# Kernel optimization log

Measured on AMD Instinct MI355X. Metric: run time of the kernel, lower is better.

The kernel has to match this reference:

```python
import jax, jax.numpy as jnp
import numpy as np

N = 100000   # nodes
E = 3200000  # edges
M = 4096     # moves
K = 16       # orders per move
NEG_SLOPE = 0.2  # PyG GATv2Conv default negative_slope

PARAM_SHAPES = {
    'g1_Wl': (10, 15), 'g1_Wr': (10, 15), 'g1_att': (10,), 'g1_b': (10,),
    'g2_Wl': (10, 25), 'g2_Wr': (10, 25), 'g2_att': (10,), 'g2_b': (10,),
    'g3_Wl': (10, 25), 'g3_Wr': (10, 25), 'g3_att': (10,), 'g3_b': (10,),
    'vt_W': (20, 29), 'vt_b': (20,), 'va_W': (1, 20), 'va_b': (1,),
    'vv_W': (10, 20), 'vv_b': (10,), 'vl_W': (1, 10), 'vl_b': (1,),
    'at_W': (20, 48), 'at_b': (20,), 'dt_W': (20, 23), 'dt_b': (20,),
    'oa_W': (1, 20), 'oa_b': (1,), 'ov_W': (1, 20), 'ov_b': (1,),
}
PARAM_NAMES = list(PARAM_SHAPES.keys())


def _linear(x, W, b):
    return x @ W.T + b


def _gatv2(x, src, dst, Wl, Wr, att, b):
    # GATv2Conv (heads=1, self-loops appended by caller), eval mode (no dropout)
    xl = x @ Wl.T  # messages from source nodes
    xr = x @ Wr.T
    e = (jax.nn.leaky_relu(xl[src] + xr[dst], NEG_SLOPE) * att).sum(-1)  # [E+N]
    emax = jax.ops.segment_max(e, dst, num_segments=N)
    ee = jnp.exp(e - emax[dst])
    denom = jax.ops.segment_sum(ee, dst, num_segments=N)
    alpha = ee / denom[dst]
    return jax.ops.segment_sum(alpha[:, None] * xl[src], dst, num_segments=N) + b


def _forward(x1, x2, edges, move_src, move_dst, move_armies, is_attack, params):
    (g1_Wl, g1_Wr, g1_att, g1_b,
     g2_Wl, g2_Wr, g2_att, g2_b,
     g3_Wl, g3_Wr, g3_att, g3_b,
     vt_W, vt_b, va_W, va_b, vv_W, vv_b, vl_W, vl_b,
     at_W, at_b, dt_W, dt_b, oa_W, oa_b, ov_W, ov_b) = params
    x2t = jnp.tile(x2, (N, 1))  # [N,4]
    self_idx = jnp.arange(N, dtype=edges.dtype)
    src = jnp.concatenate([edges[0], self_idx])
    dst = jnp.concatenate([edges[1], self_idx])
    x = jax.nn.relu(_gatv2(x1, src, dst, g1_Wl, g1_Wr, g1_att, g1_b))
    x = jax.nn.relu(_gatv2(jnp.concatenate([x, x1], 1), src, dst, g2_Wl, g2_Wr, g2_att, g2_b))
    x = jax.nn.relu(_gatv2(jnp.concatenate([x, x1], 1), src, dst, g3_Wl, g3_Wr, g3_att, g3_b))  # [N,10]
    # per-move order tensors (vectorized over [M,K]); deploy uses move_src as target
    xs, xd = x[move_src], x[move_dst]       # [M,K,10]
    x1s, x1d = x1[move_src], x1[move_dst]   # [M,K,15]
    extra = 0.6 * move_armies - 0.7 * (x1d[..., 3] + x1d[..., 4])
    attack_in = jnp.concatenate([xs, xd, x1s[..., 3:], x1d[..., 1:],
                                 move_armies[..., None], extra[..., None]], -1)  # [M,K,48]
    deploy_in = jnp.concatenate([xs, x1s[..., 3:], move_armies[..., None]], -1)  # [M,K,23]
    feat = jnp.where(is_attack[..., None] == 1,
                     _linear(attack_in, at_W, at_b),
                     _linear(deploy_in, dt_W, dt_b))
    feat = jax.nn.relu(feat)  # dropout = identity (eval)
    attn = jax.nn.softmax(_linear(feat, oa_W, oa_b), axis=1)  # softmax over orders
    p = (attn * _linear(feat, ov_W, ov_b)).sum(axis=(1, 2))   # [M]
    # value head: attention pooling over all nodes
    Vn = jax.nn.relu(_linear(jnp.concatenate([x, x1, x2t], 1), vt_W, vt_b))  # [N,20]
    vatt = jax.nn.softmax(_linear(Vn, va_W, va_b), axis=0)
    Vp = jax.nn.relu((vatt * _linear(Vn, vv_W, vv_b)).sum(axis=0))
    V = jnp.tanh(_linear(Vp, vl_W, vl_b))[0]
    return V, jax.nn.log_softmax(p, axis=0)


def setup_inputs() -> dict:
    key = jax.random.key(0)
    ks = iter(jax.random.split(key, 64))
    inp = {
        'x1': jax.random.normal(next(ks), (N, 15), jnp.float32),
        'x2': jax.random.normal(next(ks), (4,), jnp.float32),
        'edges': jax.random.randint(next(ks), (2, E), 0, N, jnp.int32),
        'move_src': jax.random.randint(next(ks), (M, K), 0, N, jnp.int32),
        'move_dst': jax.random.randint(next(ks), (M, K), 0, N, jnp.int32),
        'move_armies': jax.random.uniform(next(ks), (M, K), jnp.float32) * 10.0,
        'is_attack': jax.random.randint(next(ks), (M, K), 0, 2, jnp.int32),
    }
    for name, shape in PARAM_SHAPES.items():
        inp[name] = jax.random.normal(next(ks), shape, jnp.float32) * 0.1
    return inp


def reference(x1, x2, edges, move_src, move_dst, move_armies, is_attack,
              g1_Wl, g1_Wr, g1_att, g1_b, g2_Wl, g2_Wr, g2_att, g2_b,
              g3_Wl, g3_Wr, g3_att, g3_b, vt_W, vt_b, va_W, va_b,
              vv_W, vv_b, vl_W, vl_b, at_W, at_b, dt_W, dt_b,
              oa_W, oa_b, ov_W, ov_b):
    params = (g1_Wl, g1_Wr, g1_att, g1_b, g2_Wl, g2_Wr, g2_att, g2_b,
              g3_Wl, g3_Wr, g3_att, g3_b, vt_W, vt_b, va_W, va_b,
              vv_W, vv_b, vl_W, vl_b, at_W, at_b, dt_W, dt_b,
              oa_W, oa_b, ov_W, ov_b)
    return _forward(x1, x2, edges, move_src, move_dst, move_armies, is_attack, params)
```

## Files before the change

kernel.cpp:

```cpp
#include <hip/hip_runtime.h>
#include <hip/hip_fp16.h>
#include <math.h>

#define NN 100000
#define NE 3200000
#define MM 4096
#define KK 16
#define NEG_SLOPE 0.2f
#define SUB 8
#define BSH 8
#define NB 391
#define PCH 4096
#define FCAP 9728
#define XS 12
#define XSH 16
#define PART_BLOCKS ((NE + NN + PCH - 1) / PCH)
#define LIN_BLOCKS  ((NN + 1023) / 1024)
#define MOVE_BLOCKS ((MM * KK) / 256)
#define VAL_BLOCKS  ((NN + 255) / 256)

__device__ __forceinline__ void h10_to_f(const uint4& w0, unsigned w2, float* xs) {
    float2 f;
    f = __half22float2(*(const __half2*)&w0.x); xs[0]=f.x; xs[1]=f.y;
    f = __half22float2(*(const __half2*)&w0.y); xs[2]=f.x; xs[3]=f.y;
    f = __half22float2(*(const __half2*)&w0.z); xs[4]=f.x; xs[5]=f.y;
    f = __half22float2(*(const __half2*)&w0.w); xs[6]=f.x; xs[7]=f.y;
    f = __half22float2(*(const __half2*)&w2);   xs[8]=f.x; xs[9]=f.y;
}

__global__ __launch_bounds__(1024) void part_lin1_kernel(const int* __restrict__ edges,
                                                         int* __restrict__ cnt,
                                                         unsigned* __restrict__ recs,
                                                         const float* __restrict__ x1,
                                                         const float* __restrict__ Wl,
                                                         const float* __restrict__ Wr,
                                                         __half* __restrict__ xlh,
                                                         float* __restrict__ xr) {
    int t = threadIdx.x;
    if (blockIdx.x >= PART_BLOCKS) {
        int i = (blockIdx.x - PART_BLOCKS) * 1024 + t;
        if (i >= NN) return;
        float in[15];
        #pragma unroll
        for (int j = 0; j < 15; j++) in[j] = x1[(long)i * 15 + j];
        float sl[10];
        #pragma unroll
        for (int o = 0; o < 10; o++) {
            float l = 0.f, r = 0.f;
            #pragma unroll
            for (int j = 0; j < 15; j++) {
                l += Wl[o * 15 + j] * in[j];
                r += Wr[o * 15 + j] * in[j];
            }
            sl[o] = l;
            xr[(long)i * XS + o] = r;
        }
        unsigned u[5];
        #pragma unroll
        for (int q = 0; q < 5; q++) {
            __half2 hh = __floats2half2_rn(sl[2*q], sl[2*q+1]);
            u[q] = *(unsigned*)&hh;
        }
        uint4* p4 = (uint4*)(xlh + (long)i * XSH);
        p4[0] = make_uint4(u[0], u[1], u[2], u[3]);
        *(uint2*)(xlh + (long)i * XSH + 8) = make_uint2(u[4], 0u);
        return;
    }
    __shared__ unsigned rl[PCH];
    __shared__ unsigned srt[PCH];
    __shared__ unsigned short bb[PCH];
    __shared__ unsigned short bbs[PCH];
    __shared__ int h[NB];
    __shared__ int sc[1024];
    __shared__ int lb[NB];
    __shared__ int gb[NB];
    __shared__ int cur[NB];
    const int total = NE + NN;
    int base = blockIdx.x * PCH;
    int n = min(PCH, total - base);
    if (t < NB) { h[t] = 0; cur[t] = 0; }
    __syncthreads();
    for (int j = t; j < n; j += 1024) {
        int i = base + j;
        int s, d;
        if (i < NE) { s = edges[i]; d = edges[NE + i]; }
        else        { s = i - NE; d = s; }
        rl[j] = ((unsigned)(d & 255) << 17) | (unsigned)s;
        int b = d >> BSH;
        bb[j] = (unsigned short)b;
        atomicAdd(&h[b], 1);
    }
    __syncthreads();
    int hv = (t < NB) ? h[t] : 0;
    sc[t] = hv;
    __syncthreads();
    for (int off = 1; off < 1024; off <<= 1) {
        int v = (t >= off) ? sc[t - off] : 0;
        __syncthreads();
        sc[t] += v;
        __syncthreads();
    }
    if (t < NB) {
        lb[t] = sc[t] - hv;
        if (hv > 0) gb[t] = atomicAdd(&cnt[t], hv);
    }
    __syncthreads();
    for (int j = t; j < n; j += 1024) {
        int b = bb[j];
        int l = atomicAdd(&cur[b], 1);
        int dst = lb[b] + l;
        srt[dst] = rl[j];
        bbs[dst] = (unsigned short)b;
    }
    __syncthreads();
    for (int j = t; j < n; j += 1024) {
        int b = bbs[j];
        int pos = gb[b] + (j - lb[b]);
        if (pos < FCAP) recs[(long)b * FCAP + pos] = srt[j];
    }
}

__global__ __launch_bounds__(1024) void fine_sort_kernel(const unsigned* __restrict__ recs,
                                                         const int* __restrict__ cnt,
                                                         int* __restrict__ csr_src,
                                                         int* __restrict__ offsets) {
    __shared__ unsigned rl[FCAP];
    __shared__ int scn[512];
    __shared__ int hist[256];
    __shared__ int sc[256];
    __shared__ int hb[257];
    __shared__ int cur[256];
    int b = blockIdx.x;
    int t = threadIdx.x;
    int c = 0;
    if (t < 512) {
        c = (t < NB) ? min(cnt[t], FCAP) : 0;
        scn[t] = c;
    }
    __syncthreads();
    for (int off = 1; off < 512; off <<= 1) {
        int v = 0;
        if (t < 512 && t >= off) v = scn[t - off];
        __syncthreads();
        if (t < 512) scn[t] += v;
        __syncthreads();
    }
    int beg = (b == 0) ? 0 : scn[b - 1];
    int nb = min(cnt[b], FCAP);
    int nodebase = b << BSH;
    int nnodes = min(256, NN - nodebase);
    if (t < 256) { hist[t] = 0; cur[t] = 0; }
    __syncthreads();
    const unsigned* rsrc = recs + (long)b * FCAP;
    for (int j = t; j < nb; j += 1024) {
        unsigned r = rsrc[j];
        rl[j] = r;
        atomicAdd(&hist[r >> 17], 1);
    }
    __syncthreads();
    int hv = (t < 256) ? hist[t] : 0;
    if (t < 256) sc[t] = hv;
    __syncthreads();
    for (int off = 1; off < 256; off <<= 1) {
        int v = 0;
        if (t < 256 && t >= off) v = sc[t - off];
        __syncthreads();
        if (t < 256) sc[t] += v;
        __syncthreads();
    }
    if (t < 256) hb[t] = sc[t] - hv;
    if (t == 0) hb[256] = nb;
    __syncthreads();
    for (int j = t; j < nb; j += 1024) {
        unsigned r = rl[j];
        int l = r >> 17;
        int p = hb[l] + atomicAdd(&cur[l], 1);
        csr_src[beg + p] = (int)(r & 0x1FFFFu);
    }
    if (t < nnodes) offsets[nodebase + t] = beg + hb[t];
    if (b == NB - 1 && t == 0) offsets[NN] = beg + nb;
}

template<bool FUSE_NEXT>
__global__ void gat_aggregate_kernel(const int* __restrict__ csr_src,
                                     const int* __restrict__ offsets,
                                     const __half* __restrict__ xlh,
                                     const float* __restrict__ xr,
                                     const float* __restrict__ att,
                                     const float* __restrict__ b,
                                     const float* __restrict__ x1,
                                     const float* __restrict__ nWl,
                                     const float* __restrict__ nWr,
                                     __half* __restrict__ xlo,
                                     float* __restrict__ xro,
                                     float* __restrict__ xout)
{
    int t = blockIdx.x * blockDim.x + threadIdx.x;
    int node = t / SUB;
    int lane = t % SUB;
    if (node >= NN) return;
    float xrn[12], a[10];
    const float4* xr4 = (const float4*)(xr + (long)node * XS);
    #pragma unroll
    for (int q = 0; q < 3; q++) {
        float4 v = xr4[q];
        xrn[4*q] = v.x; xrn[4*q+1] = v.y; xrn[4*q+2] = v.z; xrn[4*q+3] = v.w;
    }
    #pragma unroll
    for (int h = 0; h < 10; h++) a[h] = att[h];
    int beg = offsets[node], end = offsets[node + 1];
    float den = 0.f, num[10];
    #pragma unroll
    for (int h = 0; h < 10; h++) num[h] = 0.f;
    int j = beg + lane;
    for (; j + 3 * SUB < end; j += 4 * SUB) {
        int s0 = csr_src[j];
        int s1 = csr_src[j + SUB];
        int s2 = csr_src[j + 2 * SUB];
        int s3 = csr_src[j + 3 * SUB];
        const __half *p0 = xlh + (long)s0 * XSH, *p1 = xlh + (long)s1 * XSH;
        const __half *p2 = xlh + (long)s2 * XSH, *p3 = xlh + (long)s3 * XSH;
        uint4 w0a = *(const uint4*)p0; unsigned w0b = *(const unsigned*)(p0 + 8);
        uint4 w1a = *(const uint4*)p1; unsigned w1b = *(const unsigned*)(p1 + 8);
        uint4 w2a = *(const uint4*)p2; unsigned w2b = *(const unsigned*)(p2 + 8);
        uint4 w3a = *(const uint4*)p3; unsigned w3b = *(const unsigned*)(p3 + 8);
        uint4 wa[4] = {w0a, w1a, w2a, w3a};
        unsigned wb[4] = {w0b, w1b, w2b, w3b};
        #pragma unroll
        for (int q = 0; q < 4; q++) {
            float xs[10];
            h10_to_f(wa[q], wb[q], xs);
            float e = 0.f;
            #pragma unroll
            for (int h = 0; h < 10; h++) {
                float v = xs[h] + xrn[h];
                v = (v >= 0.f) ? v : NEG_SLOPE * v;
                e += v * a[h];
            }
            float w = __expf(e);
            den += w;
            #pragma unroll
            for (int h = 0; h < 10; h++) num[h] += w * xs[h];
        }
    }
    for (; j < end; j += SUB) {
        int s = csr_src[j];
        const __half* ph = xlh + (long)s * XSH;
        uint4 wa = *(const uint4*)ph;
        unsigned wb = *(const unsigned*)(ph + 8);
        float xs[10];
        h10_to_f(wa, wb, xs);
        float e = 0.f;
        #pragma unroll
        for (int h = 0; h < 10; h++) {
            float v = xs[h] + xrn[h];
            v = (v >= 0.f) ? v : NEG_SLOPE * v;
            e += v * a[h];
        }
        float w = __expf(e);
        den += w;
        #pragma unroll
        for (int h = 0; h < 10; h++) num[h] += w * xs[h];
    }
    #pragma unroll
    for (int off = SUB / 2; off; off >>= 1) {
        den += __shfl_xor(den, off, SUB);
        #pragma unroll
        for (int h = 0; h < 10; h++) num[h] += __shfl_xor(num[h], off, SUB);
    }
    float inv = 1.f / den;
    float xo[10];
    #pragma unroll
    for (int h = 0; h < 10; h++) xo[h] = fmaxf(num[h] * inv + b[h], 0.f);
    if (FUSE_NEXT) {
        if (lane < 5) {
            float in2[25];
            #pragma unroll
            for (int h = 0; h < 10; h++) in2[h] = xo[h];
            #pragma unroll
            for (int h = 0; h < 15; h++) in2[10 + h] = x1[(long)node * 15 + h];
            int o0 = 2 * lane, o1 = 2 * lane + 1;
            float sl0 = 0.f, sl1 = 0.f, sr0 = 0.f, sr1 = 0.f;
            #pragma unroll
            for (int jj = 0; jj < 25; jj++) {
                sl0 += nWl[o0 * 25 + jj] * in2[jj];
                sl1 += nWl[o1 * 25 + jj] * in2[jj];
                sr0 += nWr[o0 * 25 + jj] * in2[jj];
                sr1 += nWr[o1 * 25 + jj] * in2[jj];
            }
            __half2 hp = __floats2half2_rn(sl0, sl1);
            *(unsigned*)(xlo + (long)node * XSH + o0) = *(unsigned*)&hp;
            *(float2*)(xro + (long)node * XS + o0) = make_float2(sr0, sr1);
        }
    } else {
        if (lane == 0) {
            #pragma unroll
            for (int h = 0; h < 10; h++) xout[(long)node * XS + h] = xo[h];
        }
    }
}

__global__ void move_value_kernel(const float* __restrict__ x,
                                  const float* __restrict__ x1,
                                  const float* __restrict__ x2,
                                  const int* __restrict__ msrc,
                                  const int* __restrict__ mdst,
                                  const float* __restrict__ armies,
                                  const int* __restrict__ isatk,
                                  const float* __restrict__ at_W, const float* __restrict__ at_b,
                                  const float* __restrict__ dt_W, const float* __restrict__ dt_b,
                                  const float* __restrict__ oa_W, const float* __restrict__ oa_b,
                                  const float* __restrict__ ov_W, const float* __restrict__ ov_b,
                                  const float* __restrict__ vt_W, const float* __restrict__ vt_b,
                                  const float* __restrict__ va_W, const float* __restrict__ va_b,
                                  const float* __restrict__ vv_W, const float* __restrict__ vv_b,
                                  float* __restrict__ p,
                                  float* __restrict__ partials) {
    if (blockIdx.x < MOVE_BLOCKS) {
        int t = blockIdx.x * 256 + threadIdx.x;
        int m = t >> 4;
        int k = t & 15;
        int s = msrc[t], d = mdst[t];
        float arm = armies[t];
        bool atk = (isatk[t] == 1);
        float xsrc[12];
        const float4* xs4 = (const float4*)(x + (long)s * XS);
        #pragma unroll
        for (int q = 0; q < 3; q++) {
            float4 v = xs4[q];
            xsrc[4*q]=v.x; xsrc[4*q+1]=v.y; xsrc[4*q+2]=v.z; xsrc[4*q+3]=v.w;
        }
        float feat[20];
        if (atk) {
            float in[48];
            #pragma unroll
            for (int h = 0; h < 10; h++) in[h] = xsrc[h];
            const float4* xd4 = (const float4*)(x + (long)d * XS);
            float xdst[12];
            #pragma unroll
            for (int q = 0; q < 3; q++) {
                float4 v = xd4[q];
                xdst[4*q]=v.x; xdst[4*q+1]=v.y; xdst[4*q+2]=v.z; xdst[4*q+3]=v.w;
            }
            #pragma unroll
            for (int h = 0; h < 10; h++) in[10 + h] = xdst[h];
            #pragma unroll
            for (int h = 0; h < 12; h++) in[20 + h] = x1[(long)s * 15 + 3 + h];
            #pragma unroll
            for (int h = 0; h < 14; h++) in[32 + h] = x1[(long)d * 15 + 1 + h];
            in[46] = arm;
            in[47] = 0.6f * arm - 0.7f * (x1[(long)d * 15 + 3] + x1[(long)d * 15 + 4]);
            #pragma unroll
            for (int o = 0; o < 20; o++) {
                float sum = at_b[o];
                #pragma unroll
                for (int j = 0; j < 48; j++) sum += at_W[o * 48 + j] * in[j];
                feat[o] = fmaxf(sum, 0.f);
            }
        } else {
            float in[23];
            #pragma unroll
            for (int h = 0; h < 10; h++) in[h] = xsrc[h];
            #pragma unroll
            for (int h = 0; h < 12; h++) in[10 + h] = x1[(long)s * 15 + 3 + h];
            in[22] = arm;
            #pragma unroll
            for (int o = 0; o < 20; o++) {
                float sum = dt_b[o];
                #pragma unroll
                for (int j = 0; j < 23; j++) sum += dt_W[o * 23 + j] * in[j];
                feat[o] = fmaxf(sum, 0.f);
            }
        }
        float oa = oa_b[0], ov = ov_b[0];
        #pragma unroll
        for (int j = 0; j < 20; j++) {
            oa += oa_W[j] * feat[j];
            ov += ov_W[j] * feat[j];
        }
        float mx = oa;
        #pragma unroll
        for (int off = 8; off; off >>= 1) mx = fmaxf(mx, __shfl_xor(mx, off, 16));
        float w = __expf(oa - mx);
        float nume = w * ov;
        float den = w;
        #pragma unroll
        for (int off = 8; off; off >>= 1) {
            nume += __shfl_xor(nume, off, 16);
            den  += __shfl_xor(den,  off, 16);
        }
        if (k == 0) p[m] = nume / den;
        return;
    }
    __shared__ float sm[4][11];
    int vb = blockIdx.x - MOVE_BLOCKS;
    int i = vb * 256 + threadIdx.x;
    float w = 0.f;
    float acc[10];
    #pragma unroll
    for (int h = 0; h < 10; h++) acc[h] = 0.f;
    if (i < NN) {
        float in[29];
        const float4* xi4 = (const float4*)(x + (long)i * XS);
        float xi[12];
        #pragma unroll
        for (int q = 0; q < 3; q++) {
            float4 v = xi4[q];
            xi[4*q]=v.x; xi[4*q+1]=v.y; xi[4*q+2]=v.z; xi[4*q+3]=v.w;
        }
        #pragma unroll
        for (int h = 0; h < 10; h++) in[h] = xi[h];
        #pragma unroll
        for (int h = 0; h < 15; h++) in[10 + h] = x1[(long)i * 15 + h];
        #pragma unroll
        for (int h = 0; h < 4; h++) in[25 + h] = x2[h];
        float Vn[20];
        #pragma unroll
        for (int o = 0; o < 20; o++) {
            float s = vt_b[o];
            #pragma unroll
            for (int j = 0; j < 29; j++) s += vt_W[o * 29 + j] * in[j];
            Vn[o] = fmaxf(s, 0.f);
        }
        float lg = va_b[0];
        #pragma unroll
        for (int j = 0; j < 20; j++) lg += va_W[j] * Vn[j];
        w = __expf(lg);
        #pragma unroll
        for (int o = 0; o < 10; o++) {
            float s = vv_b[o];
            #pragma unroll
            for (int j = 0; j < 20; j++) s += vv_W[o * 20 + j] * Vn[j];
            acc[o] = w * s;
        }
    }
    #pragma unroll
    for (int off = 32; off; off >>= 1) {
        w += __shfl_xor(w, off, 64);
        #pragma unroll
        for (int h = 0; h < 10; h++) acc[h] += __shfl_xor(acc[h], off, 64);
    }
    int wid = threadIdx.x >> 6;
    if ((threadIdx.x & 63) == 0) {
        #pragma unroll
        for (int h = 0; h < 10; h++) sm[wid][h] = acc[h];
        sm[wid][10] = w;
    }
    __syncthreads();
    if (threadIdx.x < 11) {
        int c = threadIdx.x;
        partials[(long)vb * 12 + c] = sm[0][c] + sm[1][c] + sm[2][c] + sm[3][c];
    }
}

__global__ void final_kernel(const float* __restrict__ p,
                             const float* __restrict__ partials,
                             const float* __restrict__ vl_W, const float* __restrict__ vl_b,
                             float* __restrict__ out) {
    if (blockIdx.x == 0) {
        __shared__ float sm[256];
        int tid = threadIdx.x;
        float mx = -INFINITY;
        for (int i = tid; i < MM; i += 256) mx = fmaxf(mx, p[i]);
        sm[tid] = mx; __syncthreads();
        for (int s = 128; s; s >>= 1) { if (tid < s) sm[tid] = fmaxf(sm[tid], sm[tid + s]); __syncthreads(); }
        mx = sm[0]; __syncthreads();
        float sum = 0.f;
        for (int i = tid; i < MM; i += 256) sum += expf(p[i] - mx);
        sm[tid] = sum; __syncthreads();
        for (int s = 128; s; s >>= 1) { if (tid < s) sm[tid] += sm[tid + s]; __syncthreads(); }
        float ls = mx + logf(sm[0]);
        for (int i = tid; i < MM; i += 256) out[1 + i] = p[i] - ls;
    } else if (threadIdx.x < 64) {
        int lane = threadIdx.x;
        float s[11];
        #pragma unroll
        for (int c = 0; c < 11; c++) s[c] = 0.f;
        for (int j = lane; j < VAL_BLOCKS; j += 64)
            #pragma unroll
            for (int c = 0; c < 11; c++) s[c] += partials[(long)j * 12 + c];
        #pragma unroll
        for (int off = 32; off; off >>= 1)
            #pragma unroll
            for (int c = 0; c < 11; c++) s[c] += __shfl_xor(s[c], off, 64);
        if (lane == 0) {
            float inv = 1.0f / s[10];
            float v = vl_b[0];
            #pragma unroll
            for (int h = 0; h < 10; h++) v += vl_W[h] * fmaxf(s[h] * inv, 0.f);
            out[0] = tanhf(v);
        }
    }
}

extern "C" void kernel_launch(void* const* d_in, const int* in_sizes, int n_in,
                              void* d_out, int out_size, void* d_ws, size_t ws_size,
                              hipStream_t stream) {
    const float* x1      = (const float*)d_in[0];
    const float* x2      = (const float*)d_in[1];
    const int*   edges   = (const int*)d_in[2];
    const int*   msrc    = (const int*)d_in[3];
    const int*   mdst    = (const int*)d_in[4];
    const float* armies  = (const float*)d_in[5];
    const int*   isatk   = (const int*)d_in[6];
    const float* g1_Wl = (const float*)d_in[7],  *g1_Wr = (const float*)d_in[8];
    const float* g1_att= (const float*)d_in[9],  *g1_b  = (const float*)d_in[10];
    const float* g2_Wl = (const float*)d_in[11], *g2_Wr = (const float*)d_in[12];
    const float* g2_att= (const float*)d_in[13], *g2_b  = (const float*)d_in[14];
    const float* g3_Wl = (const float*)d_in[15], *g3_Wr = (const float*)d_in[16];
    const float* g3_att= (const float*)d_in[17], *g3_b  = (const float*)d_in[18];
    const float* vt_W  = (const float*)d_in[19], *vt_b  = (const float*)d_in[20];
    const float* va_W  = (const float*)d_in[21], *va_b  = (const float*)d_in[22];
    const float* vv_W  = (const float*)d_in[23], *vv_b  = (const float*)d_in[24];
    const float* vl_W  = (const float*)d_in[25], *vl_b  = (const float*)d_in[26];
    const float* at_W  = (const float*)d_in[27], *at_b  = (const float*)d_in[28];
    const float* dt_W  = (const float*)d_in[29], *dt_b  = (const float*)d_in[30];
    const float* oa_W  = (const float*)d_in[31], *oa_b  = (const float*)d_in[32];
    const float* ov_W  = (const float*)d_in[33], *ov_b  = (const float*)d_in[34];

    float* out = (float*)d_out;

    float* ws = (float*)d_ws;
    __half* xlhA = (__half*)ws;
    __half* xlhB = xlhA + (long)NN * XSH;
    float* xrA = (float*)(xlhB + (long)NN * XSH);
    float* xrB = xrA + (long)NN * XS;
    float* xF  = xrB + (long)NN * XS;
    int* csr_src = (int*)(xF + (long)NN * XS);
    int* offsets = csr_src + (NE + NN);
    unsigned* recs = (unsigned*)(offsets + NN + 4);
    int* cnt   = (int*)(recs + (long)NB * FCAP);
    float* pbuf = (float*)(cnt + NB + 1);
    float* partials = pbuf + MM;

    const int aggBlocks = ((long)NN * SUB + 255) / 256;

    hipMemsetAsync(cnt, 0, NB * sizeof(int), stream);
    part_lin1_kernel<<<PART_BLOCKS + LIN_BLOCKS, 1024, 0, stream>>>(
        edges, cnt, recs, x1, g1_Wl, g1_Wr, xlhA, xrA);
    fine_sort_kernel<<<NB, 1024, 0, stream>>>(recs, cnt, csr_src, offsets);
    gat_aggregate_kernel<true><<<aggBlocks, 256, 0, stream>>>(
        csr_src, offsets, xlhA, xrA, g1_att, g1_b, x1, g2_Wl, g2_Wr, xlhB, xrB, nullptr);
    gat_aggregate_kernel<true><<<aggBlocks, 256, 0, stream>>>(
        csr_src, offsets, xlhB, xrB, g2_att, g2_b, x1, g3_Wl, g3_Wr, xlhA, xrA, nullptr);
    gat_aggregate_kernel<false><<<aggBlocks, 256, 0, stream>>>(
        csr_src, offsets, xlhA, xrA, g3_att, g3_b, x1, nullptr, nullptr, nullptr, nullptr, xF);
    move_value_kernel<<<MOVE_BLOCKS + VAL_BLOCKS, 256, 0, stream>>>(
        xF, x1, x2, msrc, mdst, armies, isatk,
        at_W, at_b, dt_W, dt_b, oa_W, oa_b, ov_W, ov_b,
        vt_W, vt_b, va_W, va_b, vv_W, vv_b, pbuf, partials);
    final_kernel<<<2, 256, 0, stream>>>(pbuf, partials, vl_W, vl_b, out);
}
```

Before: 354.9 us.

## Merge three GAT aggregation launches into one cooperative persistent kernel

```diff
diff --git a/kernel.cpp b/kernel.cpp
--- a/kernel.cpp
+++ b/kernel.cpp
@@ -1,6 +1,9 @@
 #include <hip/hip_runtime.h>
+#include <hip/hip_cooperative_groups.h>
 #include <hip/hip_fp16.h>
 #include <math.h>
+
+namespace cg = cooperative_groups;
 
 #define NN 100000
 #define NE 3200000
@@ -18,6 +21,8 @@
 #define LIN_BLOCKS  ((NN + 1023) / 1024)
 #define MOVE_BLOCKS ((MM * KK) / 256)
 #define VAL_BLOCKS  ((NN + 255) / 256)
+#define AGG_GROUPS  (((long)NN * SUB + 255) / 256)
+#define AGG_GRID    1563
 
 __device__ __forceinline__ void h10_to_f(const uint4& w0, unsigned w2, float* xs) {
     float2 f;
@@ -181,55 +186,83 @@
     if (b == NB - 1 && t == 0) offsets[NN] = beg + nb;
 }
 
+struct AggParams {
+    const int *csr_src, *offsets;
+    const float *x1;
+    const float *g1_att, *g1_b, *g2_Wl, *g2_Wr;
+    const float *g2_att, *g2_b, *g3_Wl, *g3_Wr;
+    const float *g3_att, *g3_b;
+    __half *xlhA, *xlhB; float *xrA, *xrB, *xF;
+};
+
 template<bool FUSE_NEXT>
-__global__ void gat_aggregate_kernel(const int* __restrict__ csr_src,
-                                     const int* __restrict__ offsets,
-                                     const __half* __restrict__ xlh,
-                                     const float* __restrict__ xr,
-                                     const float* __restrict__ att,
-                                     const float* __restrict__ b,
-                                     const float* __restrict__ x1,
-                                     const float* __restrict__ nWl,
-                                     const float* __restrict__ nWr,
-                                     __half* __restrict__ xlo,
-                                     float* __restrict__ xro,
-                                     float* __restrict__ xout)
-{
-    int t = blockIdx.x * blockDim.x + threadIdx.x;
-    int node = t / SUB;
-    int lane = t % SUB;
-    if (node >= NN) return;
-    float xrn[12], a[10];
-    const float4* xr4 = (const float4*)(xr + (long)node * XS);
-    #pragma unroll
-    for (int q = 0; q < 3; q++) {
-        float4 v = xr4[q];
-        xrn[4*q] = v.x; xrn[4*q+1] = v.y; xrn[4*q+2] = v.z; xrn[4*q+3] = v.w;
-    }
-    #pragma unroll
-    for (int h = 0; h < 10; h++) a[h] = att[h];
-    int beg = offsets[node], end = offsets[node + 1];
-    float den = 0.f, num[10];
-    #pragma unroll
-    for (int h = 0; h < 10; h++) num[h] = 0.f;
-    int j = beg + lane;
-    for (; j + 3 * SUB < end; j += 4 * SUB) {
-        int s0 = csr_src[j];
-        int s1 = csr_src[j + SUB];
-        int s2 = csr_src[j + 2 * SUB];
-        int s3 = csr_src[j + 3 * SUB];
-        const __half *p0 = xlh + (long)s0 * XSH, *p1 = xlh + (long)s1 * XSH;
-        const __half *p2 = xlh + (long)s2 * XSH, *p3 = xlh + (long)s3 * XSH;
-        uint4 w0a = *(const uint4*)p0; unsigned w0b = *(const unsigned*)(p0 + 8);
-        uint4 w1a = *(const uint4*)p1; unsigned w1b = *(const unsigned*)(p1 + 8);
-        uint4 w2a = *(const uint4*)p2; unsigned w2b = *(const unsigned*)(p2 + 8);
-        uint4 w3a = *(const uint4*)p3; unsigned w3b = *(const unsigned*)(p3 + 8);
-        uint4 wa[4] = {w0a, w1a, w2a, w3a};
-        unsigned wb[4] = {w0b, w1b, w2b, w3b};
-        #pragma unroll
-        for (int q = 0; q < 4; q++) {
+__device__ void aggregate_phase(const int* __restrict__ csr_src,
+                                const int* __restrict__ offsets,
+                                const __half* __restrict__ xlh,
+                                const float* __restrict__ xr,
+                                const float* __restrict__ att,
+                                const float* __restrict__ bias,
+                                const float* __restrict__ x1,
+                                const float* __restrict__ nWl,
+                                const float* __restrict__ nWr,
+                                __half* __restrict__ xlo,
+                                float* __restrict__ xro,
+                                float* __restrict__ xout) {
+    for (int g = blockIdx.x; g < AGG_GROUPS; g += AGG_GRID) {
+        int node = g * 32 + (threadIdx.x >> 3);
+        int lane = threadIdx.x & 7;
+        if (node >= NN) continue;
+        float xrn[12], a[10];
+        const float4* xr4 = (const float4*)(xr + (long)node * XS);
+        #pragma unroll
+        for (int q = 0; q < 3; q++) {
+            float4 v = xr4[q];
+            xrn[4*q] = v.x; xrn[4*q+1] = v.y; xrn[4*q+2] = v.z; xrn[4*q+3] = v.w;
+        }
+        #pragma unroll
+        for (int h = 0; h < 10; h++) a[h] = att[h];
+        int beg = offsets[node], end = offsets[node + 1];
+        float den = 0.f, num[10];
+        #pragma unroll
+        for (int h = 0; h < 10; h++) num[h] = 0.f;
+        int j = beg + lane;
+        for (; j + 3 * SUB < end; j += 4 * SUB) {
+            int s0 = csr_src[j];
+            int s1 = csr_src[j + SUB];
+            int s2 = csr_src[j + 2 * SUB];
+            int s3 = csr_src[j + 3 * SUB];
+            const __half *p0 = xlh + (long)s0 * XSH, *p1 = xlh + (long)s1 * XSH;
+            const __half *p2 = xlh + (long)s2 * XSH, *p3 = xlh + (long)s3 * XSH;
+            uint4 w0a = *(const uint4*)p0; unsigned w0b = *(const unsigned*)(p0 + 8);
+            uint4 w1a = *(const uint4*)p1; unsigned w1b = *(const unsigned*)(p1 + 8);
+            uint4 w2a = *(const uint4*)p2; unsigned w2b = *(const unsigned*)(p2 + 8);
+            uint4 w3a = *(const uint4*)p3; unsigned w3b = *(const unsigned*)(p3 + 8);
+            uint4 wa[4] = {w0a, w1a, w2a, w3a};
+            unsigned wb[4] = {w0b, w1b, w2b, w3b};
+            #pragma unroll
+            for (int q = 0; q < 4; q++) {
+                float xs[10];
+                h10_to_f(wa[q], wb[q], xs);
+                float e = 0.f;
+                #pragma unroll
+                for (int h = 0; h < 10; h++) {
+                    float v = xs[h] + xrn[h];
+                    v = (v >= 0.f) ? v : NEG_SLOPE * v;
+                    e += v * a[h];
+                }
+                float w = __expf(e);
+                den += w;
+                #pragma unroll
+                for (int h = 0; h < 10; h++) num[h] += w * xs[h];
+            }
+        }
+        for (; j < end; j += SUB) {
+            int s = csr_src[j];
+            const __half* ph = xlh + (long)s * XSH;
+            uint4 wa = *(const uint4*)ph;
+            unsigned wb = *(const unsigned*)(ph + 8);
             float xs[10];
-            h10_to_f(wa[q], wb[q], xs);
+            h10_to_f(wa, wb, xs);
             float e = 0.f;
             #pragma unroll
             for (int h = 0; h < 10; h++) {
@@ -242,62 +275,55 @@
             #pragma unroll
             for (int h = 0; h < 10; h++) num[h] += w * xs[h];
         }
-    }
-    for (; j < end; j += SUB) {
-        int s = csr_src[j];
-        const __half* ph = xlh + (long)s * XSH;
-        uint4 wa = *(const uint4*)ph;
-        unsigned wb = *(const unsigned*)(ph + 8);
-        float xs[10];
-        h10_to_f(wa, wb, xs);
-        float e = 0.f;
-        #pragma unroll
-        for (int h = 0; h < 10; h++) {
-            float v = xs[h] + xrn[h];
-            v = (v >= 0.f) ? v : NEG_SLOPE * v;
-            e += v * a[h];
-        }
-        float w = __expf(e);
-        den += w;
-        #pragma unroll
-        for (int h = 0; h < 10; h++) num[h] += w * xs[h];
-    }
-    #pragma unroll
-    for (int off = SUB / 2; off; off >>= 1) {
-        den += __shfl_xor(den, off, SUB);
-        #pragma unroll
-        for (int h = 0; h < 10; h++) num[h] += __shfl_xor(num[h], off, SUB);
-    }
-    float inv = 1.f / den;
-    float xo[10];
-    #pragma unroll
-    for (int h = 0; h < 10; h++) xo[h] = fmaxf(num[h] * inv + b[h], 0.f);
-    if (FUSE_NEXT) {
-        if (lane < 5) {
-            float in2[25];
-            #pragma unroll
-            for (int h = 0; h < 10; h++) in2[h] = xo[h];
-            #pragma unroll
-            for (int h = 0; h < 15; h++) in2[10 + h] = x1[(long)node * 15 + h];
-            int o0 = 2 * lane, o1 = 2 * lane + 1;
-            float sl0 = 0.f, sl1 = 0.f, sr0 = 0.f, sr1 = 0.f;
-            #pragma unroll
-            for (int jj = 0; jj < 25; jj++) {
-                sl0 += nWl[o0 * 25 + jj] * in2[jj];
-                sl1 += nWl[o1 * 25 + jj] * in2[jj];
-                sr0 += nWr[o0 * 25 + jj] * in2[jj];
-                sr1 += nWr[o1 * 25 + jj] * in2[jj];
-            }
-            __half2 hp = __floats2half2_rn(sl0, sl1);
-            *(unsigned*)(xlo + (long)node * XSH + o0) = *(unsigned*)&hp;
-            *(float2*)(xro + (long)node * XS + o0) = make_float2(sr0, sr1);
-        }
-    } else {
-        if (lane == 0) {
-            #pragma unroll
-            for (int h = 0; h < 10; h++) xout[(long)node * XS + h] = xo[h];
-        }
-    }
+        #pragma unroll
+        for (int off = SUB / 2; off; off >>= 1) {
+            den += __shfl_xor(den, off, SUB);
+            #pragma unroll
+            for (int h = 0; h < 10; h++) num[h] += __shfl_xor(num[h], off, SUB);
+        }
+        float inv = 1.f / den;
+        float xo[10];
+        #pragma unroll
+        for (int h = 0; h < 10; h++) xo[h] = fmaxf(num[h] * inv + bias[h], 0.f);
+        if (FUSE_NEXT) {
+            if (lane < 5) {
+                float in2[25];
+                #pragma unroll
+                for (int h = 0; h < 10; h++) in2[h] = xo[h];
+                #pragma unroll
+                for (int h = 0; h < 15; h++) in2[10 + h] = x1[(long)node * 15 + h];
+                int o0 = 2 * lane, o1 = 2 * lane + 1;
+                float sl0 = 0.f, sl1 = 0.f, sr0 = 0.f, sr1 = 0.f;
+                #pragma unroll
+                for (int jj = 0; jj < 25; jj++) {
+                    sl0 += nWl[o0 * 25 + jj] * in2[jj];
+                    sl1 += nWl[o1 * 25 + jj] * in2[jj];
+                    sr0 += nWr[o0 * 25 + jj] * in2[jj];
+                    sr1 += nWr[o1 * 25 + jj] * in2[jj];
+                }
+                __half2 hp = __floats2half2_rn(sl0, sl1);
+                *(unsigned*)(xlo + (long)node * XSH + o0) = *(unsigned*)&hp;
+                *(float2*)(xro + (long)node * XS + o0) = make_float2(sr0, sr1);
+            }
+        } else {
+            if (lane == 0) {
+                #pragma unroll
+                for (int h = 0; h < 10; h++) xout[(long)node * XS + h] = xo[h];
+            }
+        }
+    }
+}
+
+__global__ __launch_bounds__(256, 8) void agg3_kernel(AggParams P) {
+    cg::grid_group grid = cg::this_grid();
+    aggregate_phase<true>(P.csr_src, P.offsets, P.xlhA, P.xrA, P.g1_att, P.g1_b,
+                          P.x1, P.g2_Wl, P.g2_Wr, P.xlhB, P.xrB, nullptr);
+    grid.sync();
+    aggregate_phase<true>(P.csr_src, P.offsets, P.xlhB, P.xrB, P.g2_att, P.g2_b,
+                          P.x1, P.g3_Wl, P.g3_Wr, P.xlhA, P.xrA, nullptr);
+    grid.sync();
+    aggregate_phase<false>(P.csr_src, P.offsets, P.xlhA, P.xrA, P.g3_att, P.g3_b,
+                           P.x1, nullptr, nullptr, nullptr, nullptr, P.xF);
 }
 
 __global__ void move_value_kernel(const float* __restrict__ x,
@@ -533,18 +559,19 @@
     float* pbuf = (float*)(cnt + NB + 1);
     float* partials = pbuf + MM;
 
-    const int aggBlocks = ((long)NN * SUB + 255) / 256;
-
     hipMemsetAsync(cnt, 0, NB * sizeof(int), stream);
     part_lin1_kernel<<<PART_BLOCKS + LIN_BLOCKS, 1024, 0, stream>>>(
         edges, cnt, recs, x1, g1_Wl, g1_Wr, xlhA, xrA);
     fine_sort_kernel<<<NB, 1024, 0, stream>>>(recs, cnt, csr_src, offsets);
-    gat_aggregate_kernel<true><<<aggBlocks, 256, 0, stream>>>(
-        csr_src, offsets, xlhA, xrA, g1_att, g1_b, x1, g2_Wl, g2_Wr, xlhB, xrB, nullptr);
-    gat_aggregate_kernel<true><<<aggBlocks, 256, 0, stream>>>(
-        csr_src, offsets, xlhB, xrB, g2_att, g2_b, x1, g3_Wl, g3_Wr, xlhA, xrA, nullptr);
-    gat_aggregate_kernel<false><<<aggBlocks, 256, 0, stream>>>(
-        csr_src, offsets, xlhA, xrA, g3_att, g3_b, x1, nullptr, nullptr, nullptr, nullptr, xF);
+    AggParams P;
+    P.csr_src = csr_src; P.offsets = offsets; P.x1 = x1;
+    P.g1_att = g1_att; P.g1_b = g1_b; P.g2_Wl = g2_Wl; P.g2_Wr = g2_Wr;
+    P.g2_att = g2_att; P.g2_b = g2_b; P.g3_Wl = g3_Wl; P.g3_Wr = g3_Wr;
+    P.g3_att = g3_att; P.g3_b = g3_b;
+    P.xlhA = xlhA; P.xlhB = xlhB; P.xrA = xrA; P.xrB = xrB; P.xF = xF;
+    void* kargs[] = { (void*)&P };
+    hipLaunchCooperativeKernel((const void*)agg3_kernel, dim3(AGG_GRID), dim3(256),
+                               kargs, 0, stream);
     move_value_kernel<<<MOVE_BLOCKS + VAL_BLOCKS, 256, 0, stream>>>(
         xF, x1, x2, msrc, mdst, armies, isatk,
         at_W, at_b, dt_W, dt_b, oa_W, oa_b, ov_W, ov_b,
```

New measurement: 1.120 ms. 216% more time.
